# Kernel optimization log

Measured on AMD Instinct MI355X. Metric: run time of the kernel, lower is better.

## Reference

```python
import jax, jax.numpy as jnp
import numpy as np

B, P, K, L, F, KS, NCLS = 8, 4096, 20, 10, 32, 5, 40
N = B * P


def setup_inputs() -> dict:
    key = jax.random.key(0)
    k = jax.random.split(key, 5)
    return {
        "pos": jax.random.normal(k[0], (N, 3), jnp.float32),
        "Wsp": jax.random.normal(k[1], (KS ** 3, F), jnp.float32) * 0.1,
        "root": jax.random.normal(k[2], (F,), jnp.float32) * 0.1,
        "bias": jnp.zeros((F,), jnp.float32),
        "gamma": jnp.ones((F,), jnp.float32),
        "beta": jnp.zeros((F,), jnp.float32),
        "W1": jax.random.normal(k[3], (F, 256), jnp.float32) * 0.1,
        "b1": jnp.zeros((256,), jnp.float32),
        "W2": jax.random.normal(k[4], (256, NCLS), jnp.float32) * 0.1,
        "b2": jnp.zeros((NCLS,), jnp.float32),
    }


def _knn(pos):
    # per-graph brute-force knn (loop=False), neighbors sorted by distance
    pts = pos.reshape(B, P, 3)

    def one(p):
        d = jnp.sum((p[:, None, :] - p[None, :, :]) ** 2, -1)  # (P,P)
        d = d.at[jnp.arange(P), jnp.arange(P)].set(jnp.inf)
        return jax.lax.top_k(-d, K)[1]

    nbr = jax.vmap(one)(pts) + (jnp.arange(B) * P)[:, None, None]
    return nbr.reshape(N, K)


def _eig3(A):
    # power iteration with deflation (nr_iterations=5) on batched 3x3 symmetric mats
    def pi(M):
        v = jnp.full((M.shape[0], 3), np.float32(3.0 ** -0.5))
        for _ in range(5):
            v = jnp.einsum("nij,nj->ni", M, v)
            v = v / (jnp.linalg.norm(v, axis=-1, keepdims=True) + 1e-12)
        lam = jnp.einsum("ni,nij,nj->n", v, M, v)
        return lam, v

    l1, v1 = pi(A)
    _, v2 = pi(A - l1[:, None, None] * v1[:, :, None] * v1[:, None, :])
    v3 = jnp.cross(v1, v2)
    v3 = v3 / (jnp.linalg.norm(v3, axis=-1, keepdims=True) + 1e-12)
    return jnp.stack([v1, v2, v3], axis=1)  # rows = eigenvectors, V[:,2] = normal


def reference(pos, Wsp, root, bias, gamma, beta, W1, b1, W2, b2):
    nbr = _knn(pos)                               # (N,K)
    clusters = pos[nbr] - pos[:, None, :]         # (N,K,3) neighbor - center
    cov = jnp.einsum("nmc,nmd->ncd", clusters[:, :L], clusters[:, :L])
    V = _eig3(cov)                                # (N,3,3)
    dirc = jnp.einsum("nkc,ndc->nkd", clusters, V)  # clusters @ V^T
    signs = jnp.sign(dirc[:, :, 2].sum(1))
    dirc = dirc.at[:, :, 2].multiply(signs[:, None])
    max_abs = jnp.max(jnp.abs(dirc).reshape(N, -1), 1)
    dirc = dirc / max_abs[:, None, None] * 0.5 + 0.5  # pseudo coords in [0,1]

    # SplineConv, degree=1, open splines, dim=3, in_channels=1 (x=ones)
    v = dirc * (KS - 1)
    f = jnp.floor(v)
    frac = v - f
    fi = f.astype(jnp.int32)
    bits = jnp.array([[(s >> 2) & 1, (s >> 1) & 1, s & 1] for s in range(8)], jnp.int32)
    idx = jnp.clip(fi[:, :, None, :] + bits[None, None, :, :], 0, KS - 1)  # (N,K,8,3)
    wgt = jnp.where(bits[None, None] == 1, frac[:, :, None, :], 1.0 - frac[:, :, None, :])
    basis = wgt.prod(-1)                                          # (N,K,8)
    flat = (idx[..., 0] * KS + idx[..., 1]) * KS + idx[..., 2]    # (N,K,8)
    msg = jnp.einsum("nks,nksf->nf", basis, Wsp[flat]) / K        # mean aggregation
    node = msg + root + bias                                      # root weight on x=1

    # BatchNorm1d (training-mode batch stats, eps=1e-5)
    mu = node.mean(0)
    var = ((node - mu) ** 2).mean(0)
    xb = gamma * (node - mu) / jnp.sqrt(var + 1e-5) + beta

    out3 = xb[:, :, None] * V[:, 2][:, None, :]   # (N,F,3) scale normal direction
    y = jax.nn.sigmoid(out3)
    ys = y.reshape(-1, P, F).mean(1)              # (3B,F) as in torch .view
    y1 = jax.nn.elu(ys @ W1 + b1)
    return jax.nn.log_softmax(y1 @ W2 + b2, axis=1)
```

## Files before the change

### kernel.cpp

```cpp
#include <hip/hip_runtime.h>
#include <hip/hip_bf16.h>
#include <math.h>

#define BGR 8
#define PP 4096
#define NPTS 32768
#define KNN 20
#define LCOV 10
#define FF 32
#define KS 5
#define NCLS 40
#define NGROUP 24
#define GROUPLEN 131072

#define SPLIT 8
#define CHUNK (PP / SPLIT)
#define PTSBLK 128
#define KTHR 1024
#define NSLOT (KNN + 1)
#define MPAD NSLOT
#define SENT 0xFFFFFFFFu
#define SCELLS 4096
#define SCAP 12

__device__ inline unsigned umn(unsigned a, unsigned b) { return a < b ? a : b; }
__device__ inline unsigned umx(unsigned a, unsigned b) { return a > b ? a : b; }

__device__ inline void mat3vec(const float M[9], const float v[3], float w[3]) {
    w[0] = M[0] * v[0] + M[1] * v[1] + M[2] * v[2];
    w[1] = M[3] * v[0] + M[4] * v[1] + M[5] * v[2];
    w[2] = M[6] * v[0] + M[7] * v[1] + M[8] * v[2];
}

__device__ inline float pi3(const float M[9], float v[3]) {
    v[0] = v[1] = v[2] = 0.57735026918962576f;
#pragma unroll
    for (int it = 0; it < 5; ++it) {
        float w[3];
        mat3vec(M, v, w);
        float nrm = sqrtf(w[0] * w[0] + w[1] * w[1] + w[2] * w[2]) + 1e-12f;
        v[0] = w[0] / nrm;
        v[1] = w[1] / nrm;
        v[2] = w[2] / nrm;
    }
    float w[3];
    mat3vec(M, v, w);
    return v[0] * w[0] + v[1] * w[1] + v[2] * w[2];
}

__global__ __launch_bounds__(KTHR, 4) void knn_kernel(
    const float* __restrict__ pos, unsigned short* __restrict__ nbr16,
    float* __restrict__ Rbuf, float* __restrict__ v3out) {
    __shared__ float smem[4 * PP];
    __shared__ unsigned short mOrig[PP];
    __shared__ unsigned samp[PTSBLK * 24];
    __shared__ float Tseed[PTSBLK];
    __shared__ unsigned scr[KTHR / 64][SCAP][64];
    float* tx = smem;
    float* ty = smem + PP;
    float* tz = smem + 2 * PP;
    float* tw = smem + 3 * PP;
    unsigned short* lnbr = (unsigned short*)(smem + 3 * PP + 2816);

    int b = blockIdx.x >> 5;
    int blkInGraph = blockIdx.x & 31;
    const float* gp = pos + (size_t)b * PP * 3;
    int tid = threadIdx.x;

    {
        unsigned* cnt = (unsigned*)smem;
        unsigned short* cellOf = (unsigned short*)(smem + 4096);
        unsigned* tsum = (unsigned*)(smem + 6144);
        for (int i = tid; i < SCELLS; i += KTHR) cnt[i] = 0u;
        __syncthreads();
        for (int i = tid; i < PP; i += KTHR) {
            float x = gp[i * 3 + 0];
            float y = gp[i * 3 + 1];
            float z = gp[i * 3 + 2];
            int cx = min(max((int)floorf((x + 4.0f) * 2.0f), 0), 15);
            int cy = min(max((int)floorf((y + 4.0f) * 2.0f), 0), 15);
            int cz = min(max((int)floorf((z + 4.0f) * 2.0f), 0), 15);
            unsigned m = 0;
#pragma unroll
            for (int bb = 0; bb < 4; ++bb)
                m |= (((unsigned)(cx >> bb) & 1u) << (3 * bb + 2)) |
                     (((unsigned)(cy >> bb) & 1u) << (3 * bb + 1)) |
                     (((unsigned)(cz >> bb) & 1u) << (3 * bb + 0));
            cellOf[i] = (unsigned short)m;
            atomicAdd(&cnt[m], 1u);
        }
        __syncthreads();
        unsigned c0 = cnt[4 * tid + 0];
        unsigned c1 = cnt[4 * tid + 1];
        unsigned c2 = cnt[4 * tid + 2];
        unsigned c3 = cnt[4 * tid + 3];
        unsigned local = c0 + c1 + c2 + c3;
        tsum[tid] = local;
        __syncthreads();
        for (int off = 1; off < 1024; off <<= 1) {
            unsigned v = (tid >= off) ? tsum[tid - off] : 0u;
            __syncthreads();
            tsum[tid] += v;
            __syncthreads();
        }
        unsigned base = tsum[tid] - local;
        cnt[4 * tid + 0] = base;
        cnt[4 * tid + 1] = base + c0;
        cnt[4 * tid + 2] = base + c0 + c1;
        cnt[4 * tid + 3] = base + c0 + c1 + c2;
        __syncthreads();
        for (int i = tid; i < PP; i += KTHR) {
            unsigned dst = atomicAdd(&cnt[cellOf[i]], 1u);
            mOrig[dst] = (unsigned short)i;
        }
    }
    __syncthreads();

    for (int i = tid; i < PP; i += KTHR) {
        float x = gp[i * 3 + 0];
        float y = gp[i * 3 + 1];
        float z = gp[i * 3 + 2];
        tx[i] = -2.0f * x;
        ty[i] = -2.0f * y;
        tz[i] = -2.0f * z;
        tw[i] = x * x + y * y + z * z;
    }
    __syncthreads();

    int eighth = tid >> 7;
    int pt = tid & (PTSBLK - 1);
    int lane = tid & 63;
    int qSlot = blkInGraph * PTSBLK + pt;
    int li = mOrig[qSlot];
    float px = -0.5f * tx[li];
    float py = -0.5f * ty[li];
    float pz = -0.5f * tz[li];
    float p2 = tw[li];
    int jbeg = eighth * CHUNK;

    {
        unsigned s0 = SENT, s1 = SENT, s2 = SENT;
#pragma unroll 4
        for (int c = 0; c < 24; ++c) {
            int base = jbeg + c * 20;
            float4 xv = *(const float4*)(tx + base);
            float4 yv = *(const float4*)(ty + base);
            float4 zv = *(const float4*)(tz + base);
            float4 wv = *(const float4*)(tw + base);
            float xa[4] = {xv.x, xv.y, xv.z, xv.w};
            float ya[4] = {yv.x, yv.y, yv.z, yv.w};
            float za[4] = {zv.x, zv.y, zv.z, zv.w};
            float wa[4] = {wv.x, wv.y, wv.z, wv.w};
#pragma unroll
            for (int u = 0; u < 4; ++u) {
                float dh = fmaf(px, xa[u], fmaf(py, ya[u], fmaf(pz, za[u], wa[u])));
                float d = fmaxf(dh + p2, 0.0f);
                unsigned key = (__float_as_uint(d) & 0xFFFFF000u)
                               | (unsigned)(base + u);
                if (base + u == li) key = SENT;
                unsigned t0 = umn(key, s0); key = umx(key, s0); s0 = t0;
                t0 = umn(key, s1); key = umx(key, s1); s1 = t0;
                s2 = umn(key, s2);
            }
        }
        unsigned* sdst = &samp[pt * 24 + eighth * 3];
        sdst[0] = s0; sdst[1] = s1; sdst[2] = s2;
    }
    __syncthreads();
    if (tid < PTSBLK) {
        unsigned g0 = 0, g1 = 0, g2 = 0, g3 = 0;
        const unsigned* ss = &samp[tid * 24];
#pragma unroll
        for (int i = 0; i < 24; ++i) {
            unsigned k = ss[i], a;
            a = umx(k, g0); k = umn(k, g0); g0 = a;
            a = umx(k, g1); k = umn(k, g1); g1 = a;
            a = umx(k, g2); k = umn(k, g2); g2 = a;
            g3 = umx(k, g3);
        }
        Tseed[tid] = __uint_as_float((g3 & 0xFFFFF000u) + 0x2000u);
    }
    __syncthreads();
    float seed_hat = Tseed[pt] - p2;

    unsigned bd[NSLOT];
#pragma unroll
    for (int k = 0; k < NSLOT; k++) bd[k] = SENT;
    float worst_hat = seed_hat;

    unsigned* scrW = &scr[tid >> 6][0][0];
    unsigned cnt = 0;

    auto drain = [&]() {
#pragma unroll
        for (int s = 0; s < SCAP; ++s) {
            if (!__any((int)cnt > s)) break;
            unsigned k = (s < (int)cnt) ? scrW[s * 64 + lane] : SENT;
#pragma unroll
            for (int i = 0; i < NSLOT; i++) {
                unsigned lo = umn(k, bd[i]);
                k = umx(k, bd[i]);
                bd[i] = lo;
            }
        }
        cnt = 0;
        unsigned wb = bd[NSLOT - 1];
        float nw = (wb == SENT) ? INFINITY
                                : __uint_as_float(wb & 0xFFFFF000u) - p2;
        worst_hat = fminf(nw, seed_hat);
    };

    for (int jj = jbeg; jj < jbeg + CHUNK; jj += 8) {
        float4 xv0 = *(const float4*)(tx + jj);
        float4 yv0 = *(const float4*)(ty + jj);
        float4 zv0 = *(const float4*)(tz + jj);
        float4 wv0 = *(const float4*)(tw + jj);
        float4 xv1 = *(const float4*)(tx + jj + 4);
        float4 yv1 = *(const float4*)(ty + jj + 4);
        float4 zv1 = *(const float4*)(tz + jj + 4);
        float4 wv1 = *(const float4*)(tw + jj + 4);
        float xa[8] = {xv0.x, xv0.y, xv0.z, xv0.w, xv1.x, xv1.y, xv1.z, xv1.w};
        float ya[8] = {yv0.x, yv0.y, yv0.z, yv0.w, yv1.x, yv1.y, yv1.z, yv1.w};
        float za[8] = {zv0.x, zv0.y, zv0.z, zv0.w, zv1.x, zv1.y, zv1.z, zv1.w};
        float wa[8] = {wv0.x, wv0.y, wv0.z, wv0.w, wv1.x, wv1.y, wv1.z, wv1.w};
#pragma unroll
        for (int u = 0; u < 8; u++) {
            float dh = fmaf(px, xa[u], fmaf(py, ya[u], fmaf(pz, za[u], wa[u])));
            if (dh < worst_hat) {
                float d = fmaxf(dh + p2, 0.0f);
                scrW[cnt * 64 + lane] = (__float_as_uint(d) & 0xFFFFF000u)
                                        | (unsigned)(jj + u);
                cnt++;
            }
        }
        if (__any(cnt >= 4u)) drain();
    }
    drain();

    __syncthreads();
    unsigned* mk = (unsigned*)smem;
    for (int h = 0; h < 2; h++) {
        if ((pt >> 6) == h) {
            int lpt = pt & 63;
#pragma unroll
            for (int k = 0; k < NSLOT; k++)
                mk[(eighth * 64 + lpt) * MPAD + k] = bd[k];
        }
        __syncthreads();
        if (tid < 64) {
            int p = tid;
            const unsigned* base = &mk[p * MPAD];
            int cur[SPLIT];
#pragma unroll
            for (int q = 0; q < SPLIT; q++) cur[q] = 0;
            int lpt2 = h * 64 + p;
            int gi = b * PP + (int)mOrig[blkInGraph * PTSBLK + lpt2];
#pragma unroll
            for (int t = 0; t < NSLOT; t++) {
                unsigned v[SPLIT];
#pragma unroll
                for (int q = 0; q < SPLIT; q++)
                    v[q] = base[q * 64 * MPAD + cur[q]];
                unsigned m = v[0];
#pragma unroll
                for (int q = 1; q < SPLIT; q++) m = umn(m, v[q]);
                if (t > 0) {
                    int local = (int)(m & 0xFFFu);
                    nbr16[(size_t)gi * KNN + (t - 1)] = (unsigned short)local;
                    lnbr[lpt2 * KNN + (t - 1)] = (unsigned short)local;
                }
#pragma unroll
                for (int q = 0; q < SPLIT; q++) cur[q] += (v[q] == m);
            }
        }
        __syncthreads();
    }

    for (int i = tid; i < PP; i += KTHR) {
        tx[i] = gp[i * 3 + 0];
        ty[i] = gp[i * 3 + 1];
        tz[i] = gp[i * 3 + 2];
    }
    __syncthreads();

    if (tid < PTSBLK) {
        int lp = tid;
        int ng = mOrig[blkInGraph * PTSBLK + lp];
        int n = b * PP + ng;
        float qx = tx[ng], qy = ty[ng], qz = tz[ng];
        const unsigned short* ln = &lnbr[lp * KNN];

        float m00 = 0.f, m01 = 0.f, m02 = 0.f, m11 = 0.f, m12 = 0.f, m22 = 0.f;
#pragma unroll
        for (int k = 0; k < LCOV; k++) {
            int id = ln[k];
            float cx = tx[id] - qx;
            float cy = ty[id] - qy;
            float cz = tz[id] - qz;
            m00 += cx * cx; m01 += cx * cy; m02 += cx * cz;
            m11 += cy * cy; m12 += cy * cz; m22 += cz * cz;
        }
        float M[9] = {m00, m01, m02, m01, m11, m12, m02, m12, m22};

        float v1[3], v2[3], v3[3];
        float l1 = pi3(M, v1);
        float M2[9];
#pragma unroll
        for (int c = 0; c < 3; c++)
#pragma unroll
            for (int d = 0; d < 3; d++)
                M2[c * 3 + d] = M[c * 3 + d] - l1 * v1[c] * v1[d];
        pi3(M2, v2);
        v3[0] = v1[1] * v2[2] - v1[2] * v2[1];
        v3[1] = v1[2] * v2[0] - v1[0] * v2[2];
        v3[2] = v1[0] * v2[1] - v1[1] * v2[0];
        {
            float nrm = sqrtf(v3[0] * v3[0] + v3[1] * v3[1] + v3[2] * v3[2]) + 1e-12f;
            v3[0] /= nrm; v3[1] /= nrm; v3[2] /= nrm;
        }

        float ssum = 0.f, mx = 0.f;
#pragma unroll
        for (int k = 0; k < KNN; k++) {
            int id = ln[k];
            float cx = tx[id] - qx;
            float cy = ty[id] - qy;
            float cz = tz[id] - qz;
            float d0 = cx * v1[0] + cy * v1[1] + cz * v1[2];
            float d1 = cx * v2[0] + cy * v2[1] + cz * v2[2];
            float d2 = cx * v3[0] + cy * v3[1] + cz * v3[2];
            ssum += d2;
            mx = fmaxf(mx, fabsf(d0));
            mx = fmaxf(mx, fabsf(d1));
            mx = fmaxf(mx, fabsf(d2));
        }
        float sgn = (ssum > 0.f) ? 1.f : ((ssum < 0.f) ? -1.f : 0.f);

        float sc = 2.0f / mx;
        float* R = Rbuf + (size_t)n * 12;
        R[0] = v1[0] * sc;  R[1] = v1[1] * sc;  R[2] = v1[2] * sc;
        R[3] = v2[0] * sc;  R[4] = v2[1] * sc;  R[5] = v2[2] * sc;
        float s2 = sgn * sc;
        R[6] = v3[0] * s2;  R[7] = v3[1] * s2;  R[8] = v3[2] * s2;
        R[9] = 0.f; R[10] = 0.f; R[11] = 0.f;

        v3out[n * 3 + 0] = v3[0];
        v3out[n * 3 + 1] = v3[1];
        v3out[n * 3 + 2] = v3[2];
    }
}

#define NPB 16
#define SPLBLKS (NPTS / NPB)
__global__ __launch_bounds__(512) void spline_kernel(
    const float* __restrict__ pos, const unsigned short* __restrict__ nbr16,
    const float* __restrict__ Rbuf, const float* __restrict__ Wsp,
    const float* __restrict__ root, const float* __restrict__ bias,
    float* __restrict__ node, float* __restrict__ sums_part) {
    __shared__ float wbuf[NPB * KNN * 8];

    int tid = threadIdx.x;
    if (tid < NPB * KNN) {
        int pt = tid / KNN;
        int k = tid - pt * KNN;
        int n = blockIdx.x * NPB + pt;
        const float4* Rv = (const float4*)(Rbuf + (size_t)n * 12);
        float4 r0 = Rv[0], r1 = Rv[1], r2 = Rv[2];
        float px = pos[n * 3 + 0], py = pos[n * 3 + 1], pz = pos[n * 3 + 2];
        int id = (n & ~(PP - 1)) | (int)nbr16[(size_t)n * KNN + k];
        float cxx = pos[id * 3 + 0] - px;
        float cyy = pos[id * 3 + 1] - py;
        float czz = pos[id * 3 + 2] - pz;
        float v0 = fmaf(cxx, r0.x, fmaf(cyy, r0.y, fmaf(czz, r0.z, 2.0f)));
        float v1 = fmaf(cxx, r0.w, fmaf(cyy, r1.x, fmaf(czz, r1.y, 2.0f)));
        float v2 = fmaf(cxx, r1.z, fmaf(cyy, r1.w, fmaf(czz, r2.x, 2.0f)));
        float f0 = floorf(v0), f1 = floorf(v1), f2 = floorf(v2);
        float fr0 = v0 - f0, fr1 = v1 - f1, fr2 = v2 - f2;
        int fi0 = (int)f0, fi1 = (int)f1, fi2 = (int)f2;
        float* wdst = &wbuf[(pt * KNN + k) * 8];
#pragma unroll
        for (int s = 0; s < 8; s++) {
            int b0 = (s >> 2) & 1, b1 = (s >> 1) & 1, b2s = s & 1;
            int i0 = min(max(fi0 + b0, 0), KS - 1);
            int i1 = min(max(fi1 + b1, 0), KS - 1);
            int i2 = min(max(fi2 + b2s, 0), KS - 1);
            float w = (b0 ? fr0 : 1.f - fr0) * (b1 ? fr1 : 1.f - fr1) *
                      (b2s ? fr2 : 1.f - fr2);
            unsigned flat = (unsigned)((i0 * KS + i1) * KS + i2);
            wdst[s] = __uint_as_float((__float_as_uint(w) & ~127u) | flat);
        }
    }
    __syncthreads();

    int pt = tid >> 5;
    int f = tid & 31;
    const float* wrow = &wbuf[pt * (KNN * 8)];
    float acc = 0.f;
#pragma unroll
    for (int k = 0; k < KNN; k++) {
        float4 wa = *(const float4*)&wrow[k * 8];
        float4 wb = *(const float4*)&wrow[k * 8 + 4];
        float wv[8] = {wa.x, wa.y, wa.z, wa.w, wb.x, wb.y, wb.z, wb.w};
#pragma unroll
        for (int s = 0; s < 8; s++) {
            unsigned u = __float_as_uint(wv[s]) & 127u;
            acc = fmaf(wv[s], Wsp[u * FF + f], acc);
        }
    }
    int n = blockIdx.x * NPB + pt;
    float val = acc * (1.0f / KNN) + root[f] + bias[f];
    node[(size_t)n * FF + f] = val;

    __syncthreads();
    wbuf[tid] = val;
    wbuf[512 + tid] = val * val;
    __syncthreads();
    if (tid < 64) {
        int ff = tid & 31;
        int off = (tid >> 5) * 512;
        float s = 0.f;
#pragma unroll
        for (int p = 0; p < NPB; p++) s += wbuf[off + p * 32 + ff];
        sums_part[(size_t)blockIdx.x * 64 + tid] = s;
    }
}

#define YSPLIT 8
#define YCHUNK (GROUPLEN / YSPLIT)
__global__ __launch_bounds__(256) void ys_kernel(
    const float* __restrict__ node, const float* __restrict__ v3,
    const float* __restrict__ sums_part, const float* __restrict__ gamma,
    const float* __restrict__ beta, float* __restrict__ ys_part) {
    __shared__ float stat4[256];
    __shared__ float stat[64];
    __shared__ float sa[FF], sb[FF];
    {
        int col = threadIdx.x & 63;
        int q = threadIdx.x >> 6;
        float s0 = 0.f, s1 = 0.f, s2 = 0.f, s3 = 0.f;
        for (int p = q * 512; p < (q + 1) * 512; p += 4) {
            s0 += sums_part[(p + 0) * 64 + col];
            s1 += sums_part[(p + 1) * 64 + col];
            s2 += sums_part[(p + 2) * 64 + col];
            s3 += sums_part[(p + 3) * 64 + col];
        }
        stat4[threadIdx.x] = (s0 + s1) + (s2 + s3);
    }
    __syncthreads();
    if (threadIdx.x < 64) {
        stat[threadIdx.x] = stat4[threadIdx.x] + stat4[64 + threadIdx.x] +
                            stat4[128 + threadIdx.x] + stat4[192 + threadIdx.x];
    }
    __syncthreads();
    if (threadIdx.x < FF) {
        int f = threadIdx.x;
        float mu = stat[f] * (1.0f / NPTS);
        float var = stat[FF + f] * (1.0f / NPTS) - mu * mu;
        float inv = 1.0f / sqrtf(var + 1e-5f);
        sa[f] = gamma[f] * inv;
        sb[f] = beta[f] - gamma[f] * inv * mu;
    }
    __syncthreads();

    int g = blockIdx.x >> 3;
    int sub = blockIdx.x & 7;
    int t0 = g * GROUPLEN + sub * YCHUNK + threadIdx.x;
    int n = t0 / 96;
    int r0 = t0 - n * 96;
    int rj[3], fj[3], cj[3], dj[3];
    rj[0] = r0;
    rj[1] = (r0 + 64) % 96;
    rj[2] = (r0 + 32) % 96;
#pragma unroll
    for (int j = 0; j < 3; j++) {
        fj[j] = rj[j] / 3;
        cj[j] = rj[j] - fj[j] * 3;
        dj[j] = (rj[j] >= 32) ? 3 : 2;
    }
    float Sa0 = sa[fj[0]], Sb0 = sb[fj[0]];
    float Sa1 = sa[fj[1]], Sb1 = sb[fj[1]];
    float Sa2 = sa[fj[2]], Sb2 = sb[fj[2]];
    int nf = n * FF;
    int n3 = n * 3;

    float acc = 0.f;
#pragma unroll 1
    for (int tr = 0; tr < 21; tr++) {
        {
            float xb = fmaf(Sa0, node[nf + fj[0]], Sb0);
            float val = xb * v3[n3 + cj[0]];
            acc += 1.0f / (1.0f + __expf(-val));
            nf += dj[0] * FF; n3 += dj[0] * 3;
        }
        {
            float xb = fmaf(Sa1, node[nf + fj[1]], Sb1);
            float val = xb * v3[n3 + cj[1]];
            acc += 1.0f / (1.0f + __expf(-val));
            nf += dj[1] * FF; n3 += dj[1] * 3;
        }
        {
            float xb = fmaf(Sa2, node[nf + fj[2]], Sb2);
            float val = xb * v3[n3 + cj[2]];
            acc += 1.0f / (1.0f + __expf(-val));
            nf += dj[2] * FF; n3 += dj[2] * 3;
        }
    }
    {
        float xb = fmaf(Sa0, node[nf + fj[0]], Sb0);
        float val = xb * v3[n3 + cj[0]];
        acc += 1.0f / (1.0f + __expf(-val));
    }

    __shared__ float red[256];
    red[threadIdx.x] = acc;
    __syncthreads();
    if (threadIdx.x < FF) {
        float s = 0.f;
        for (int t = threadIdx.x; t < 256; t += FF) s += red[t];
        ys_part[(sub * NGROUP + g) * FF + threadIdx.x] = s * (1.0f / PP);
    }
}

__global__ __launch_bounds__(256) void head_kernel(
    const float* __restrict__ ys_part, const float* __restrict__ W1,
    const float* __restrict__ b1, const float* __restrict__ W2,
    const float* __restrict__ b2, float* __restrict__ out) {
    int g = blockIdx.x;
    __shared__ float syr[FF];
    __shared__ float h[256];
    __shared__ float logits[NCLS];
    __shared__ float mstat[2];
    if (threadIdx.x < FF) {
        float s = 0.f;
#pragma unroll
        for (int sub = 0; sub < YSPLIT; sub++)
            s += ys_part[(sub * NGROUP + g) * FF + threadIdx.x];
        syr[threadIdx.x] = s;
    }
    __syncthreads();
    int j = threadIdx.x;
    float acc = b1[j];
#pragma unroll
    for (int f = 0; f < FF; f++) acc += syr[f] * W1[f * 256 + j];
    h[j] = acc > 0.f ? acc : expm1f(acc);
    __syncthreads();
    if (j < NCLS) {
        float l = b2[j];
        for (int q = 0; q < 256; q++) l += h[q] * W2[q * NCLS + j];
        logits[j] = l;
    }
    __syncthreads();
    if (j == 0) {
        float m = -INFINITY;
        for (int o = 0; o < NCLS; o++) m = fmaxf(m, logits[o]);
        float s = 0.f;
        for (int o = 0; o < NCLS; o++) s += expf(logits[o] - m);
        mstat[0] = m;
        mstat[1] = logf(s);
    }
    __syncthreads();
    if (j < NCLS) out[g * NCLS + j] = logits[j] - mstat[0] - mstat[1];
}

extern "C" void kernel_launch(void* const* d_in, const int* in_sizes, int n_in,
                              void* d_out, int out_size, void* d_ws, size_t ws_size,
                              hipStream_t stream) {
    const float* pos   = (const float*)d_in[0];
    const float* Wsp   = (const float*)d_in[1];
    const float* root  = (const float*)d_in[2];
    const float* bias  = (const float*)d_in[3];
    const float* gamma = (const float*)d_in[4];
    const float* beta  = (const float*)d_in[5];
    const float* W1    = (const float*)d_in[6];
    const float* b1    = (const float*)d_in[7];
    const float* W2    = (const float*)d_in[8];
    const float* b2    = (const float*)d_in[9];
    float* out = (float*)d_out;

    char* ws = (char*)d_ws;
    unsigned short* nbr16 = (unsigned short*)(ws);
    float* sums_part = (float*)(ws + 1310720);
    float* ys_part   = (float*)(ws + 1835008);
    float* node = (float*)(ws + 2621440);
    float* v3   = (float*)(ws + 6815744);
    float* Rbuf = (float*)(ws + 7212288);

    knn_kernel<<<256, KTHR, 0, stream>>>(pos, nbr16, Rbuf, v3);
    spline_kernel<<<SPLBLKS, 512, 0, stream>>>(pos, nbr16, Rbuf, Wsp, root,
                                               bias, node, sums_part);
    ys_kernel<<<NGROUP * YSPLIT, 256, 0, stream>>>(node, v3, sums_part, gamma,
                                                   beta, ys_part);
    head_kernel<<<NGROUP, 256, 0, stream>>>(ys_part, W1, b1, W2, b2, out);
}
```

Measured before the change: 203.1 us.

## Use wave-shuffle prefix scan, denser seed sampling, and double-buffered LDS loads in kNN scan

Replaces the 10-step block-wide LDS Hillis-Steele scan, which needed two barriers per step, with a two-level wavefront shuffle scan needing only two barriers. The seed sampling now takes 32 contiguous 16-point groups instead of 24 groups at stride 20, aiming for a tighter initial pruning threshold. The main distance loop software-pipelines its shared-memory float4 loads (A/B double buffering) so LDS latency overlaps the compare/insert work. This adds register pressure in a kernel already launched with 1024 threads at bounds 4.

```diff
diff --git a/kernel.cpp b/kernel.cpp
--- a/kernel.cpp
+++ b/kernel.cpp
@@ -56,6 +56,7 @@
     __shared__ unsigned samp[PTSBLK * 24];
     __shared__ float Tseed[PTSBLK];
     __shared__ unsigned scr[KTHR / 64][SCAP][64];
+    __shared__ unsigned wsum[16];
     float* tx = smem;
     float* ty = smem + PP;
     float* tz = smem + 2 * PP;
@@ -66,11 +67,12 @@
     int blkInGraph = blockIdx.x & 31;
     const float* gp = pos + (size_t)b * PP * 3;
     int tid = threadIdx.x;
+    int lane = tid & 63;
+    int wid = tid >> 6;
 
     {
         unsigned* cnt = (unsigned*)smem;
         unsigned short* cellOf = (unsigned short*)(smem + 4096);
-        unsigned* tsum = (unsigned*)(smem + 6144);
         for (int i = tid; i < SCELLS; i += KTHR) cnt[i] = 0u;
         __syncthreads();
         for (int i = tid; i < PP; i += KTHR) {
@@ -95,15 +97,26 @@
         unsigned c2 = cnt[4 * tid + 2];
         unsigned c3 = cnt[4 * tid + 3];
         unsigned local = c0 + c1 + c2 + c3;
-        tsum[tid] = local;
+        unsigned v = local;
+#pragma unroll
+        for (int off = 1; off < 64; off <<= 1) {
+            unsigned o = __shfl_up(v, off);
+            if (lane >= off) v += o;
+        }
+        if (lane == 63) wsum[wid] = v;
         __syncthreads();
-        for (int off = 1; off < 1024; off <<= 1) {
-            unsigned v = (tid >= off) ? tsum[tid - off] : 0u;
-            __syncthreads();
-            tsum[tid] += v;
-            __syncthreads();
-        }
-        unsigned base = tsum[tid] - local;
+        if (tid < 64) {
+            unsigned w = (tid < 16) ? wsum[tid] : 0u;
+            unsigned vv = w;
+#pragma unroll
+            for (int off = 1; off < 16; off <<= 1) {
+                unsigned o = __shfl_up(vv, off);
+                if (tid >= off) vv += o;
+            }
+            if (tid < 16) wsum[tid] = vv - w;
+        }
+        __syncthreads();
+        unsigned base = wsum[wid] + (v - local);
         cnt[4 * tid + 0] = base;
         cnt[4 * tid + 1] = base + c0;
         cnt[4 * tid + 2] = base + c0 + c1;
@@ -129,7 +142,6 @@
 
     int eighth = tid >> 7;
     int pt = tid & (PTSBLK - 1);
-    int lane = tid & 63;
     int qSlot = blkInGraph * PTSBLK + pt;
     int li = mOrig[qSlot];
     float px = -0.5f * tx[li];
@@ -141,8 +153,8 @@
     {
         unsigned s0 = SENT, s1 = SENT, s2 = SENT;
 #pragma unroll 4
-        for (int c = 0; c < 24; ++c) {
-            int base = jbeg + c * 20;
+        for (int c = 0; c < 32; ++c) {
+            int base = jbeg + c * 16;
             float4 xv = *(const float4*)(tx + base);
             float4 yv = *(const float4*)(ty + base);
             float4 zv = *(const float4*)(tz + base);
@@ -188,7 +200,7 @@
     for (int k = 0; k < NSLOT; k++) bd[k] = SENT;
     float worst_hat = seed_hat;
 
-    unsigned* scrW = &scr[tid >> 6][0][0];
+    unsigned* scrW = &scr[wid][0][0];
     unsigned cnt = 0;
 
     auto drain = [&]() {
@@ -210,15 +222,8 @@
         worst_hat = fminf(nw, seed_hat);
     };
 
-    for (int jj = jbeg; jj < jbeg + CHUNK; jj += 8) {
-        float4 xv0 = *(const float4*)(tx + jj);
-        float4 yv0 = *(const float4*)(ty + jj);
-        float4 zv0 = *(const float4*)(tz + jj);
-        float4 wv0 = *(const float4*)(tw + jj);
-        float4 xv1 = *(const float4*)(tx + jj + 4);
-        float4 yv1 = *(const float4*)(ty + jj + 4);
-        float4 zv1 = *(const float4*)(tz + jj + 4);
-        float4 wv1 = *(const float4*)(tw + jj + 4);
+    auto eval8 = [&](int jj, float4 xv0, float4 yv0, float4 zv0, float4 wv0,
+                     float4 xv1, float4 yv1, float4 zv1, float4 wv1) {
         float xa[8] = {xv0.x, xv0.y, xv0.z, xv0.w, xv1.x, xv1.y, xv1.z, xv1.w};
         float ya[8] = {yv0.x, yv0.y, yv0.z, yv0.w, yv1.x, yv1.y, yv1.z, yv1.w};
         float za[8] = {zv0.x, zv0.y, zv0.z, zv0.w, zv1.x, zv1.y, zv1.z, zv1.w};
@@ -234,6 +239,38 @@
             }
         }
         if (__any(cnt >= 4u)) drain();
+    };
+
+    {
+        float4 Ax0 = *(const float4*)(tx + jbeg);
+        float4 Ay0 = *(const float4*)(ty + jbeg);
+        float4 Az0 = *(const float4*)(tz + jbeg);
+        float4 Aw0 = *(const float4*)(tw + jbeg);
+        float4 Ax1 = *(const float4*)(tx + jbeg + 4);
+        float4 Ay1 = *(const float4*)(ty + jbeg + 4);
+        float4 Az1 = *(const float4*)(tz + jbeg + 4);
+        float4 Aw1 = *(const float4*)(tw + jbeg + 4);
+        for (int jj = jbeg; jj < jbeg + CHUNK; jj += 16) {
+            float4 Bx0 = *(const float4*)(tx + jj + 8);
+            float4 By0 = *(const float4*)(ty + jj + 8);
+            float4 Bz0 = *(const float4*)(tz + jj + 8);
+            float4 Bw0 = *(const float4*)(tw + jj + 8);
+            float4 Bx1 = *(const float4*)(tx + jj + 12);
+            float4 By1 = *(const float4*)(ty + jj + 12);
+            float4 Bz1 = *(const float4*)(tz + jj + 12);
+            float4 Bw1 = *(const float4*)(tw + jj + 12);
+            eval8(jj, Ax0, Ay0, Az0, Aw0, Ax1, Ay1, Az1, Aw1);
+            int nx = (jj + 16 < jbeg + CHUNK) ? jj + 16 : jbeg;
+            Ax0 = *(const float4*)(tx + nx);
+            Ay0 = *(const float4*)(ty + nx);
+            Az0 = *(const float4*)(tz + nx);
+            Aw0 = *(const float4*)(tw + nx);
+            Ax1 = *(const float4*)(tx + nx + 4);
+            Ay1 = *(const float4*)(ty + nx + 4);
+            Az1 = *(const float4*)(tz + nx + 4);
+            Aw1 = *(const float4*)(tw + nx + 4);
+            eval8(jj + 8, Bx0, By0, Bz0, Bw0, Bx1, By1, Bz1, Bw1);
+        }
     }
     drain();
 
```

New measurement: 411.3 us. 103% more time.
